# Kernel tuning notes

Measured on AMD Instinct MI355X. Metric: run time of the kernel, lower is better.

## Reference

```python
import jax, jax.numpy as jnp
import numpy as np

DECAY = 0.99
EPS = 1e-05
B, C, H, W = 64, 64, 64, 64   # C == embedding_dim
K = 512                       # num_embedding


def setup_inputs() -> dict:
    key = jax.random.key(0)
    k1, k2 = jax.random.split(key)
    inp = jax.random.normal(k1, (B, C, H, W), dtype=jnp.float32)
    embedding = jax.random.normal(k2, (C, K), dtype=jnp.float32)
    cluster_size = jnp.zeros((K,), dtype=jnp.float32)
    embedding_avg = embedding  # buffer initialized as a clone of embedding
    return {"input": inp, "embedding": embedding,
            "cluster_size": cluster_size, "embedding_avg": embedding_avg}


def reference(input, embedding, cluster_size, embedding_avg):
    # NCHW -> NHWC, flatten to [N, C]
    x = jnp.transpose(input, (0, 2, 3, 1))           # [B,H,W,C]
    flat = x.reshape(-1, embedding.shape[0])          # [N,C]
    # squared L2 distances to all K codes: [N,K]
    dist = (jnp.sum(flat * flat, axis=1, keepdims=True)
            - 2.0 * flat @ embedding
            + jnp.sum(embedding * embedding, axis=0, keepdims=True))
    ind = jnp.argmin(dist, axis=1)                    # [N] int
    # gather codes (uses OLD embedding, as in torch)
    quantize = jnp.take(embedding.T, ind, axis=0).reshape(x.shape)  # [B,H,W,C]
    # EMA updates (training branch). Avoid materializing one-hot:
    counts = jnp.zeros((K,), dtype=flat.dtype).at[ind].add(1.0)      # onehot.sum(0)
    embedding_sum = jax.ops.segment_sum(flat, ind, num_segments=K).T  # [C,K] == flat.T @ onehot
    new_cluster_size = cluster_size * DECAY + (1.0 - DECAY) * counts
    new_embedding_avg = embedding_avg * DECAY + (1.0 - DECAY) * embedding_sum
    n = jnp.sum(new_cluster_size)
    cs = (new_cluster_size + EPS) / (n + K * EPS) * n
    new_embedding = new_embedding_avg / cs[None, :]
    # commitment loss and straight-through estimator
    diff = jnp.mean((jax.lax.stop_gradient(quantize) - x) ** 2)
    quantize_st = x + jax.lax.stop_gradient(quantize - x)
    out = jnp.transpose(quantize_st, (0, 3, 1, 2))    # back to NCHW
    embedding_ind = ind.reshape(x.shape[:-1])         # [B,H,W]
    return out, diff, embedding_ind, new_embedding, new_cluster_size, new_embedding_avg
```

## Files before the change

### kernel.cpp

```cpp
#include <hip/hip_runtime.h>
#include <cstdint>
#include <cstddef>

typedef _Float16 half4v __attribute__((ext_vector_type(4)));
typedef _Float16 half8v __attribute__((ext_vector_type(8)));
typedef float    f32x4  __attribute__((ext_vector_type(4)));

#define N_PTS   262144
#define CDIM    64
#define KCODES  512
#define TAUA    5e-3f
#define FLAG_CAP 65536u

#define OFF_DIFF 16777216u
#define OFF_IND  16777217u
#define OFF_EMB  17039361u
#define OFF_CSZ  17072129u
#define OFF_AVG  17072641u

__global__ __launch_bounds__(512) void k_main(
    const float* __restrict__ in, const float* __restrict__ emb,
    float* __restrict__ out,
    int* __restrict__ ind_buf, float* __restrict__ diff_acc,
    unsigned* __restrict__ nflag, int* __restrict__ flaglist)
{
    __shared__ __align__(16) char bsm[133120];
    float* ee2_lds = (float*)(bsm + 131072);
    const int tid = threadIdx.x;

    {
        const int col = tid;
        const int xr  = (col & 7) << 4;
        float s = 0.f;
        #pragma unroll
        for (int c0 = 0; c0 < CDIM; c0 += 4) {
            float v[4];
            #pragma unroll
            for (int i = 0; i < 4; ++i) v[i] = emb[(c0 + i)*KCODES + col];
            half4v h, lo;
            #pragma unroll
            for (int i = 0; i < 4; ++i) {
                s = fmaf(v[i], v[i], s);
                _Float16 hh = (_Float16)v[i];
                h[i]  = hh;
                lo[i] = (_Float16)(v[i] - (float)hh);
            }
            const int wb = col*128 + ((c0*2) ^ xr);
            *(half4v*)(bsm + wb)         = h;
            *(half4v*)(bsm + 65536 + wb) = lo;
        }
        ee2_lds[col] = 0.5f * s;
    }
    __syncthreads();

    const int w  = tid >> 6, l = tid & 63;
    const int g  = l >> 4,  lc = l & 15;

    for (int r = 0; r < 2; ++r) {
        const int pbase = (blockIdx.x << 10) + (r << 9) + (w << 6);
        const int b     = pbase >> 12;
        const float* inb = in + ((size_t)b << 18) + ((pbase & 4095) + lc);

        half8v ah[4][2], al[4][2];
        float xs = 0.f;
        #pragma unroll
        for (int t = 0; t < 4; ++t)
            #pragma unroll
            for (int s = 0; s < 2; ++s)
                #pragma unroll
                for (int j = 0; j < 8; ++j) {
                    const int c = s*32 + g*8 + j;
                    const float x = inb[(size_t)c*4096 + t*16];
                    xs = fmaf(x, x, xs);
                    const float xf = -x;
                    const _Float16 hh = (_Float16)xf;
                    ah[t][s][j] = hh;
                    al[t][s][j] = (_Float16)(xf - (float)hh);
                }

        float d1[4][4], d2[4][4]; int k1[4][4];
        #pragma unroll
        for (int t = 0; t < 4; ++t)
            #pragma unroll
            for (int rr = 0; rr < 4; ++rr) { d1[t][rr] = 3.4e38f; d2[t][rr] = 3.4e38f; k1[t][rr] = 0; }

        for (int ct = 0; ct < 32; ++ct) {
            const int col  = (ct << 4) + lc;
            const float sd = ee2_lds[col];
            const int rb   = col*128 + ((g*16) ^ ((col & 7) << 4));
            half8v bh0 = *(const half8v*)(bsm + rb);
            half8v bh1 = *(const half8v*)(bsm + (rb ^ 64));
            half8v bl0 = *(const half8v*)(bsm + 65536 + rb);
            half8v bl1 = *(const half8v*)(bsm + 65536 + (rb ^ 64));

            #pragma unroll
            for (int t = 0; t < 4; ++t) {
                f32x4 acc0 = {sd, sd, sd, sd};
                f32x4 acc1 = {0.f, 0.f, 0.f, 0.f};
                acc0 = __builtin_amdgcn_mfma_f32_16x16x32_f16(al[t][0], bh0, acc0, 0, 0, 0);
                acc1 = __builtin_amdgcn_mfma_f32_16x16x32_f16(al[t][1], bh1, acc1, 0, 0, 0);
                acc0 = __builtin_amdgcn_mfma_f32_16x16x32_f16(ah[t][0], bl0, acc0, 0, 0, 0);
                acc1 = __builtin_amdgcn_mfma_f32_16x16x32_f16(ah[t][1], bl1, acc1, 0, 0, 0);
                acc0 = __builtin_amdgcn_mfma_f32_16x16x32_f16(ah[t][0], bh0, acc0, 0, 0, 0);
                acc1 = __builtin_amdgcn_mfma_f32_16x16x32_f16(ah[t][1], bh1, acc1, 0, 0, 0);
                #pragma unroll
                for (int rr = 0; rr < 4; ++rr) {
                    const float d = acc0[rr] + acc1[rr];
                    const bool cc = d < d1[t][rr];
                    d2[t][rr] = fminf(d2[t][rr], fmaxf(d, d1[t][rr]));
                    d1[t][rr] = fminf(d1[t][rr], d);
                    k1[t][rr] = cc ? col : k1[t][rr];
                }
            }
        }

        #pragma unroll
        for (int m = 1; m <= 8; m <<= 1) {
            #pragma unroll
            for (int t = 0; t < 4; ++t)
                #pragma unroll
                for (int rr = 0; rr < 4; ++rr) {
                    const float od1 = __shfl_xor(d1[t][rr], m);
                    const int   ok1 = __shfl_xor(k1[t][rr], m);
                    const float od2 = __shfl_xor(d2[t][rr], m);
                    const float nd2 = fminf(fmaxf(d1[t][rr], od1), fminf(d2[t][rr], od2));
                    const bool take = (od1 < d1[t][rr]) || (od1 == d1[t][rr] && ok1 < k1[t][rr]);
                    d1[t][rr] = take ? od1 : d1[t][rr];
                    k1[t][rr] = take ? ok1 : k1[t][rr];
                    d2[t][rr] = nd2;
                }
        }

        float ds = 0.f;
        if (lc == 0) {
            #pragma unroll
            for (int t = 0; t < 4; ++t) {
                const int nb = pbase + t*16 + (g << 2);
                int4 iv = make_int4(k1[t][0], k1[t][1], k1[t][2], k1[t][3]);
                *(int4*)(ind_buf + nb) = iv;
                #pragma unroll
                for (int rr = 0; rr < 4; ++rr) {
                    out[OFF_IND + nb + rr] = (float)k1[t][rr];
                    ds += d1[t][rr];
                    if (d2[t][rr] - d1[t][rr] < TAUA) {
                        unsigned ix = atomicAdd(nflag, 1u);
                        if (ix < FLAG_CAP) flaglist[ix] = nb + rr;
                    }
                }
            }
        }
        #pragma unroll
        for (int m = 1; m < 64; m <<= 1) {
            ds += __shfl_xor(ds, m);
            xs += __shfl_xor(xs, m);
        }
        if (l == 0) atomicAdd(diff_acc, 2.f*ds + xs);
    }
}

__global__ void k_refine(const float* __restrict__ in, const float* __restrict__ emb,
                         const unsigned* __restrict__ nflag, const int* __restrict__ flaglist,
                         int* __restrict__ ind_buf, float* __restrict__ out)
{
    const int gtid = blockIdx.x*blockDim.x + threadIdx.x;
    const int wid  = gtid >> 6;
    const int lane = threadIdx.x & 63;
    const int nw   = (gridDim.x * blockDim.x) >> 6;
    unsigned nf = *nflag; if (nf > FLAG_CAP) nf = FLAG_CAP;
    for (unsigned f = wid; f < nf; f += nw) {
        const int n = flaglist[f];
        const int b = n >> 12, hw = n & 4095;
        const float* xb = in + ((size_t)b << 18) + hw;
        const float* er = emb + lane*8;
        double dd[8] = {0,0,0,0,0,0,0,0};
        for (int c = 0; c < CDIM; ++c) {
            const double xv = (double)xb[(size_t)c << 12];
            #pragma unroll
            for (int j = 0; j < 8; ++j) {
                double t = xv - (double)er[c*KCODES + j];
                dd[j] = fma(t, t, dd[j]);
            }
        }
        double bd = 1e300; int bk = 0;
        #pragma unroll
        for (int j = 0; j < 8; ++j) {
            const int kk = lane*8 + j;
            if (dd[j] < bd) { bd = dd[j]; bk = kk; }
        }
        for (int off = 32; off; off >>= 1) {
            double od = __shfl_xor(bd, off);
            int    ok = __shfl_xor(bk, off);
            if (od < bd || (od == bd && ok < bk)) { bd = od; bk = ok; }
        }
        if (lane == 0) { ind_buf[n] = bk; out[OFF_IND + n] = (float)bk; }
    }
}

__global__ __launch_bounds__(512) void k_stats(const float* __restrict__ in,
    const int* __restrict__ ind_buf, float* __restrict__ p_sum, float* __restrict__ p_cnt)
{
    __shared__ __align__(16) char xsm[2][CDIM*128];
    __shared__ int   ind_lds[2][32];
    __shared__ float s_cnt[KCODES];

    const int tid = threadIdx.x;
    const int wg  = blockIdx.x;
    const int n0  = wg << 10;
    const int b   = n0 >> 12;
    const float* inb = in + ((size_t)b << 18) + (n0 & 4095);

    for (int i = tid; i < KCODES; i += 512) s_cnt[i] = 0.f;

    const int sc  = tid >> 3;
    const int sp  = (tid & 7) << 2;
    const int sxr = (sc & 7) << 4;
    const int wb_hi = sc*128 + ((sp*2)      ^ sxr);
    const int wb_lo = sc*128 + ((64 + sp*2) ^ sxr);

    const int w  = tid >> 6, l = tid & 63;
    const int g  = l >> 4,  lc = l & 15;
    const int k0w = w << 6;

    f32x4 acc[4][4];
    #pragma unroll
    for (int ci = 0; ci < 4; ++ci)
        #pragma unroll
        for (int kt = 0; kt < 4; ++kt) acc[ci][kt] = (f32x4){0.f, 0.f, 0.f, 0.f};

    {
        const float4 xv = *(const float4*)(inb + (size_t)sc*4096 + sp);
        half4v h, lo;
        #pragma unroll
        for (int i = 0; i < 4; ++i) {
            const float x = ((const float*)&xv)[i];
            _Float16 hh = (_Float16)x;
            h[i] = hh; lo[i] = (_Float16)(x - (float)hh);
        }
        *(half4v*)(&xsm[0][0] + wb_hi) = h;
        *(half4v*)(&xsm[0][0] + wb_lo) = lo;
        if (tid < 8) *(int4*)&ind_lds[0][tid*4] = *(const int4*)(ind_buf + n0 + tid*4);
    }

    for (int t = 0; t < 32; ++t) {
        __syncthreads();
        float4 nxt; int4 niv;
        if (t < 31) {
            nxt = *(const float4*)(inb + (size_t)sc*4096 + (t+1)*32 + sp);
            if (tid < 8) niv = *(const int4*)(ind_buf + n0 + (t+1)*32 + tid*4);
        }
        if (tid < 32) atomicAdd(&s_cnt[ind_lds[t & 1][tid]], 1.f);

        const char* xb = &xsm[t & 1][0];
        half8v ah[4], al[4];
        #pragma unroll
        for (int ci = 0; ci < 4; ++ci) {
            const int c  = (ci << 4) + lc;
            const int xr = (c & 7) << 4;
            ah[ci] = *(const half8v*)(xb + c*128 + ((g*16)      ^ xr));
            al[ci] = *(const half8v*)(xb + c*128 + ((64 + g*16) ^ xr));
        }
        int idv[8];
        *(int4*)&idv[0] = *(const int4*)&ind_lds[t & 1][g*8];
        *(int4*)&idv[4] = *(const int4*)&ind_lds[t & 1][g*8 + 4];
        #pragma unroll
        for (int kt = 0; kt < 4; ++kt) {
            const int tgt = k0w + (kt << 4) + lc;
            half8v bf;
            #pragma unroll
            for (int j = 0; j < 8; ++j) bf[j] = (idv[j] == tgt) ? (_Float16)1.0f : (_Float16)0.0f;
            #pragma unroll
            for (int ci = 0; ci < 4; ++ci) {
                acc[ci][kt] = __builtin_amdgcn_mfma_f32_16x16x32_f16(ah[ci], bf, acc[ci][kt], 0, 0, 0);
                acc[ci][kt] = __builtin_amdgcn_mfma_f32_16x16x32_f16(al[ci], bf, acc[ci][kt], 0, 0, 0);
            }
        }
        if (t < 31) {
            half4v h, lo;
            #pragma unroll
            for (int i = 0; i < 4; ++i) {
                const float x = ((const float*)&nxt)[i];
                _Float16 hh = (_Float16)x;
                h[i] = hh; lo[i] = (_Float16)(x - (float)hh);
            }
            char* xn = &xsm[(t+1) & 1][0];
            *(half4v*)(xn + wb_hi) = h;
            *(half4v*)(xn + wb_lo) = lo;
            if (tid < 8) *(int4*)&ind_lds[(t+1) & 1][tid*4] = niv;
        }
    }
    __syncthreads();

    float* ps = p_sum + (size_t)wg * (CDIM*KCODES);
    #pragma unroll
    for (int ci = 0; ci < 4; ++ci)
        #pragma unroll
        for (int kt = 0; kt < 4; ++kt)
            #pragma unroll
            for (int rr = 0; rr < 4; ++rr)
                ps[((ci << 4) + (g << 2) + rr)*KCODES + k0w + (kt << 4) + lc] = acc[ci][kt][rr];
    float* pc = p_cnt + wg * KCODES;
    for (int i = tid; i < KCODES; i += 512) pc[i] = s_cnt[i];
}

__global__ __launch_bounds__(256) void k_reduce1(const float* __restrict__ p_sum,
    const float* __restrict__ p_cnt, float* __restrict__ partial8,
    float* __restrict__ cnt8, int wsl)
{
    const int ic = blockIdx.x & 31, ws = blockIdx.x >> 5;
    const int i4 = ic*1024 + threadIdx.x*4;
    const float* base = p_sum + (size_t)ws*wsl*(CDIM*KCODES) + i4;
    float4 s = make_float4(0.f, 0.f, 0.f, 0.f);
    for (int w = 0; w < wsl; ++w) {
        const float4 v = *(const float4*)(base + (size_t)w*(CDIM*KCODES));
        s.x += v.x; s.y += v.y; s.z += v.z; s.w += v.w;
    }
    *(float4*)(partial8 + ws*(CDIM*KCODES) + i4) = s;
    if (ic == 0) {
        for (int k = threadIdx.x; k < KCODES; k += 256) {
            float c = 0.f;
            for (int w = 0; w < wsl; ++w) c += p_cnt[(ws*wsl + w)*KCODES + k];
            cnt8[ws*KCODES + k] = c;
        }
    }
}

__global__ __launch_bounds__(256) void k_reduce2(const float* __restrict__ partial8,
    const float* __restrict__ cnt8, float* __restrict__ sum_tot, float* __restrict__ cnt_tot)
{
    const int i4 = (blockIdx.x*256 + threadIdx.x)*4;
    float4 s = make_float4(0.f, 0.f, 0.f, 0.f);
    #pragma unroll
    for (int p = 0; p < 8; ++p) {
        const float4 v = *(const float4*)(partial8 + p*(CDIM*KCODES) + i4);
        s.x += v.x; s.y += v.y; s.z += v.z; s.w += v.w;
    }
    *(float4*)(sum_tot + i4) = s;
    if (blockIdx.x == 0) {
        for (int k = threadIdx.x; k < KCODES; k += 256) {
            float c = 0.f;
            #pragma unroll
            for (int p = 0; p < 8; ++p) c += cnt8[p*KCODES + k];
            cnt_tot[k] = c;
        }
    }
}

__global__ __launch_bounds__(512) void k_scalars(const float* __restrict__ csz,
    const float* __restrict__ cnt_tot, const float* __restrict__ diff_acc,
    float* __restrict__ out, float* __restrict__ cs_ws)
{
    __shared__ float red[512];
    const int k = threadIdx.x;
    const float ncs = csz[k]*0.99f + 0.01f*cnt_tot[k];
    out[OFF_CSZ + k] = ncs;
    red[k] = ncs;
    __syncthreads();
    for (int s = 256; s > 0; s >>= 1) { if (k < s) red[k] += red[k+s]; __syncthreads(); }
    const float n = red[0];
    cs_ws[k] = (ncs + 1e-5f) / (n + 0.00512f) * n;
    if (k == 0) out[OFF_DIFF] = diff_acc[0] * (1.f/16777216.f);
}

__global__ void k_emb(const float* __restrict__ eavg, const float* __restrict__ sum_tot,
                      const float* __restrict__ cs_ws, float* __restrict__ out)
{
    const int i = blockIdx.x*blockDim.x + threadIdx.x;
    const float avg = eavg[i]*0.99f + 0.01f*sum_tot[i];
    out[OFF_AVG + i] = avg;
    out[OFF_EMB + i] = avg / cs_ws[i & (KCODES-1)];
}

__global__ void k_quant(const float* __restrict__ emb, const int* __restrict__ ind_buf,
                        float* __restrict__ out)
{
    const int gid = blockIdx.x*blockDim.x + threadIdx.x;
    const int i  = gid << 2;
    const int hw = i & 4095;
    const int c  = (i >> 12) & 63;
    const int b  = i >> 18;
    const int n  = (b << 12) + hw;
    const int4 iv = *(const int4*)(ind_buf + n);
    const float* er = emb + (c << 9);
    float4 o = make_float4(er[iv.x], er[iv.y], er[iv.z], er[iv.w]);
    *(float4*)(out + i) = o;
}

extern "C" void kernel_launch(void* const* d_in, const int* in_sizes, int n_in,
                              void* d_out, int out_size, void* d_ws, size_t ws_size,
                              hipStream_t stream)
{
    const float* in   = (const float*)d_in[0];
    const float* emb  = (const float*)d_in[1];
    const float* csz  = (const float*)d_in[2];
    const float* eavg = (const float*)d_in[3];
    float* out = (float*)d_out;
    char* ws = (char*)d_ws;

    int*      ind      = (int*)(ws + 2048);
    float*    diff_acc = (float*)(ws + 1050624);
    unsigned* nflag    = (unsigned*)(ws + 1050640);
    int*      flaglist = (int*)(ws + 1050656);
    float*    cs_ws    = (float*)(ws + 1312800);
    float*    cnt_tot  = (float*)(ws + 1314848);
    float*    sum_tot  = (float*)(ws + 1316896);
    const size_t off_part = 1447968;
    const int swgs = 256;
    float* p_sum    = (float*)(ws + off_part);
    float* p_cnt    = (float*)(ws + off_part + (size_t)swgs*(CDIM*KCODES)*4);
    float* partial8 = (float*)(ws + off_part + (size_t)swgs*133120);
    float* cnt8     = (float*)(ws + off_part + (size_t)swgs*133120 + 1048576);

    hipMemsetAsync(ws + 1050624, 0, 32, stream);

    hipLaunchKernelGGL(k_main,    dim3(256),   dim3(512), 0, stream, in, emb, out, ind, diff_acc, nflag, flaglist);
    hipLaunchKernelGGL(k_refine,  dim3(256),   dim3(256), 0, stream, in, emb, nflag, flaglist, ind, out);
    hipLaunchKernelGGL(k_stats,   dim3(256),   dim3(512), 0, stream, in, ind, p_sum, p_cnt);
    hipLaunchKernelGGL(k_reduce1, dim3(256),   dim3(256), 0, stream, p_sum, p_cnt, partial8, cnt8, swgs >> 3);
    hipLaunchKernelGGL(k_reduce2, dim3(32),    dim3(256), 0, stream, partial8, cnt8, sum_tot, cnt_tot);
    hipLaunchKernelGGL(k_scalars, dim3(1),     dim3(512), 0, stream, csz, cnt_tot, diff_acc, out, cs_ws);
    hipLaunchKernelGGL(k_emb,     dim3(128),   dim3(256), 0, stream, eavg, sum_tot, cs_ws, out);
    hipLaunchKernelGGL(k_quant,   dim3(16384), dim3(256), 0, stream, emb, ind, out);
}
```

Before: 216.3 us.

## Fuse quantize gather into main/refine kernels and drop fp16 lo-split in stats

Removes the separate k_quant launch. The main kernel now stages its argmin indices in shared memory and writes the quantized NCHW output directly from the codebook. The refine kernel rewrites the output for any points whose index it corrects. Separately, k_stats stops splitting x into fp16 hi/lo halves, which halves the MFMA count and LDS traffic for embedding_sum at the cost of fp16 precision in that sum. There is a risk that the refine overwrite races with the main kernel's stores, but the two are ordered on the stream.

```diff
diff --git a/kernel.cpp b/kernel.cpp
--- a/kernel.cpp
+++ b/kernel.cpp
@@ -25,6 +25,7 @@
     unsigned* __restrict__ nflag, int* __restrict__ flaglist)
 {
     __shared__ __align__(16) char bsm[133120];
+    __shared__ __align__(16) int ind_sh[1024];
     float* ee2_lds = (float*)(bsm + 131072);
     const int tid = threadIdx.x;
 
@@ -138,6 +139,7 @@
                 const int nb = pbase + t*16 + (g << 2);
                 int4 iv = make_int4(k1[t][0], k1[t][1], k1[t][2], k1[t][3]);
                 *(int4*)(ind_buf + nb) = iv;
+                *(int4*)&ind_sh[(r << 9) + (w << 6) + t*16 + (g << 2)] = iv;
                 #pragma unroll
                 for (int rr = 0; rr < 4; ++rr) {
                     out[OFF_IND + nb + rr] = (float)k1[t][rr];
@@ -155,6 +157,24 @@
             xs += __shfl_xor(xs, m);
         }
         if (l == 0) atomicAdd(diff_acc, 2.f*ds + xs);
+    }
+
+    __syncthreads();
+    {
+        const int n0  = blockIdx.x << 10;
+        const int bq  = n0 >> 12;
+        const int hw0 = n0 & 4095;
+        float* outb = out + ((size_t)bq << 18) + hw0;
+        #pragma unroll 4
+        for (int it = 0; it < 32; ++it) {
+            const int idx = it*512 + tid;
+            const int c   = idx >> 8;
+            const int p4  = (idx & 255) << 2;
+            const int4 iv = *(const int4*)&ind_sh[p4];
+            const float* er = emb + (c << 9);
+            float4 o = make_float4(er[iv.x], er[iv.y], er[iv.z], er[iv.w]);
+            *(float4*)(outb + ((size_t)c << 12) + p4) = o;
+        }
     }
 }
 
@@ -193,6 +213,7 @@
             if (od < bd || (od == bd && ok < bk)) { bd = od; bk = ok; }
         }
         if (lane == 0) { ind_buf[n] = bk; out[OFF_IND + n] = (float)bk; }
+        out[((size_t)b << 18) + ((size_t)lane << 12) + hw] = emb[(lane << 9) + bk];
     }
 }
 
@@ -214,8 +235,7 @@
     const int sc  = tid >> 3;
     const int sp  = (tid & 7) << 2;
     const int sxr = (sc & 7) << 4;
-    const int wb_hi = sc*128 + ((sp*2)      ^ sxr);
-    const int wb_lo = sc*128 + ((64 + sp*2) ^ sxr);
+    const int wb_hi = sc*128 + ((sp*2) ^ sxr);
 
     const int w  = tid >> 6, l = tid & 63;
     const int g  = l >> 4,  lc = l & 15;
@@ -229,15 +249,10 @@
 
     {
         const float4 xv = *(const float4*)(inb + (size_t)sc*4096 + sp);
-        half4v h, lo;
-        #pragma unroll
-        for (int i = 0; i < 4; ++i) {
-            const float x = ((const float*)&xv)[i];
-            _Float16 hh = (_Float16)x;
-            h[i] = hh; lo[i] = (_Float16)(x - (float)hh);
-        }
+        half4v h;
+        #pragma unroll
+        for (int i = 0; i < 4; ++i) h[i] = (_Float16)(((const float*)&xv)[i]);
         *(half4v*)(&xsm[0][0] + wb_hi) = h;
-        *(half4v*)(&xsm[0][0] + wb_lo) = lo;
         if (tid < 8) *(int4*)&ind_lds[0][tid*4] = *(const int4*)(ind_buf + n0 + tid*4);
     }
 
@@ -251,13 +266,12 @@
         if (tid < 32) atomicAdd(&s_cnt[ind_lds[t & 1][tid]], 1.f);
 
         const char* xb = &xsm[t & 1][0];
-        half8v ah[4], al[4];
+        half8v ah[4];
         #pragma unroll
         for (int ci = 0; ci < 4; ++ci) {
             const int c  = (ci << 4) + lc;
             const int xr = (c & 7) << 4;
-            ah[ci] = *(const half8v*)(xb + c*128 + ((g*16)      ^ xr));
-            al[ci] = *(const half8v*)(xb + c*128 + ((64 + g*16) ^ xr));
+            ah[ci] = *(const half8v*)(xb + c*128 + ((g*16) ^ xr));
         }
         int idv[8];
         *(int4*)&idv[0] = *(const int4*)&ind_lds[t & 1][g*8];
@@ -269,22 +283,14 @@
             #pragma unroll
             for (int j = 0; j < 8; ++j) bf[j] = (idv[j] == tgt) ? (_Float16)1.0f : (_Float16)0.0f;
             #pragma unroll
-            for (int ci = 0; ci < 4; ++ci) {
+            for (int ci = 0; ci < 4; ++ci)
                 acc[ci][kt] = __builtin_amdgcn_mfma_f32_16x16x32_f16(ah[ci], bf, acc[ci][kt], 0, 0, 0);
-                acc[ci][kt] = __builtin_amdgcn_mfma_f32_16x16x32_f16(al[ci], bf, acc[ci][kt], 0, 0, 0);
-            }
         }
         if (t < 31) {
-            half4v h, lo;
-            #pragma unroll
-            for (int i = 0; i < 4; ++i) {
-                const float x = ((const float*)&nxt)[i];
-                _Float16 hh = (_Float16)x;
-                h[i] = hh; lo[i] = (_Float16)(x - (float)hh);
-            }
-            char* xn = &xsm[(t+1) & 1][0];
-            *(half4v*)(xn + wb_hi) = h;
-            *(half4v*)(xn + wb_lo) = lo;
+            half4v h;
+            #pragma unroll
+            for (int i = 0; i < 4; ++i) h[i] = (_Float16)(((const float*)&nxt)[i]);
+            *(half4v*)(&xsm[(t+1) & 1][0] + wb_hi) = h;
             if (tid < 8) *(int4*)&ind_lds[(t+1) & 1][tid*4] = niv;
         }
     }
@@ -368,21 +374,6 @@
     const float avg = eavg[i]*0.99f + 0.01f*sum_tot[i];
     out[OFF_AVG + i] = avg;
     out[OFF_EMB + i] = avg / cs_ws[i & (KCODES-1)];
-}
-
-__global__ void k_quant(const float* __restrict__ emb, const int* __restrict__ ind_buf,
-                        float* __restrict__ out)
-{
-    const int gid = blockIdx.x*blockDim.x + threadIdx.x;
-    const int i  = gid << 2;
-    const int hw = i & 4095;
-    const int c  = (i >> 12) & 63;
-    const int b  = i >> 18;
-    const int n  = (b << 12) + hw;
-    const int4 iv = *(const int4*)(ind_buf + n);
-    const float* er = emb + (c << 9);
-    float4 o = make_float4(er[iv.x], er[iv.y], er[iv.z], er[iv.w]);
-    *(float4*)(out + i) = o;
 }
 
 extern "C" void kernel_launch(void* const* d_in, const int* in_sizes, int n_in,
@@ -419,5 +410,4 @@
     hipLaunchKernelGGL(k_reduce2, dim3(32),    dim3(256), 0, stream, partial8, cnt8, sum_tot, cnt_tot);
     hipLaunchKernelGGL(k_scalars, dim3(1),     dim3(512), 0, stream, csz, cnt_tot, diff_acc, out, cs_ws);
     hipLaunchKernelGGL(k_emb,     dim3(128),   dim3(256), 0, stream, eavg, sum_tot, cs_ws, out);
-    hipLaunchKernelGGL(k_quant,   dim3(16384), dim3(256), 0, stream, emb, ind, out);
-}
+}
```

Result: slower. 221.5 us (+2.4%).
